# Performance work log

Measured on AMD Instinct MI355X. Metric: run time of the kernel, lower is better.

## Reference

```python
import jax, jax.numpy as jnp
import numpy as np

N_NODES = 100000
N_EDGES = 1600000
IN_DIM = 128
HIDDEN = 128
N_GRAPHS = 256


def setup_inputs() -> dict:
    key = jax.random.key(0)
    ks = jax.random.split(key, 12)
    x = jax.random.normal(ks[0], (N_NODES, IN_DIM), dtype=jnp.float32)
    edge_index = jax.random.randint(ks[1], (2, N_EDGES), 0, N_NODES, dtype=jnp.int64)
    batch = jnp.sort(jax.random.randint(ks[2], (N_NODES,), 0, N_GRAPHS, dtype=jnp.int64))
    s = 0.05
    W1 = jax.random.normal(ks[3], (IN_DIM, HIDDEN), dtype=jnp.float32) * s
    b1 = jnp.zeros((HIDDEN,), dtype=jnp.float32)
    W2 = jax.random.normal(ks[4], (HIDDEN, HIDDEN), dtype=jnp.float32) * s
    b2 = jnp.zeros((HIDDEN,), dtype=jnp.float32)
    W3 = jax.random.normal(ks[5], (HIDDEN, HIDDEN), dtype=jnp.float32) * s
    b3 = jnp.zeros((HIDDEN,), dtype=jnp.float32)
    Wh = jax.random.normal(ks[6], (HIDDEN, 2), dtype=jnp.float32) * s
    bh = jnp.zeros((2,), dtype=jnp.float32)
    return {"x": x, "edge_index": edge_index, "batch": batch,
            "W1": W1, "b1": b1, "W2": W2, "b2": b2, "W3": W3, "b3": b3,
            "Wh": Wh, "bh": bh}


def _gcn_structure(edge_index, n_nodes):
    # PyG GCNConv default: add self-loops, symmetric deg^-1/2 normalization.
    loop = jnp.arange(n_nodes, dtype=edge_index.dtype)
    src = jnp.concatenate([edge_index[0], loop])  # message source j
    dst = jnp.concatenate([edge_index[1], loop])  # aggregate at i
    deg = jax.ops.segment_sum(jnp.ones_like(dst, dtype=jnp.float32), dst,
                              num_segments=n_nodes)
    dinv = jnp.where(deg > 0, jax.lax.rsqrt(deg), 0.0)
    norm = dinv[src] * dinv[dst]  # [E + N]
    return src, dst, norm


def _gcn_conv(x, W, b, src, dst, norm, n_nodes):
    h = x @ W  # dense transform first (PyG order)
    msg = h[src] * norm[:, None]  # gather + per-edge scale
    agg = jax.ops.segment_sum(msg, dst, num_segments=n_nodes)  # scatter-add
    return agg + b


def reference(x, edge_index, batch, W1, b1, W2, b2, W3, b3, Wh, bh):
    n = x.shape[0]
    src, dst, norm = _gcn_structure(edge_index, n)
    # dropout is a no-op in eval mode (training=False)
    h = jax.nn.relu(_gcn_conv(x, W1, b1, src, dst, norm, n))
    h = jax.nn.relu(_gcn_conv(h, W2, b2, src, dst, norm, n))
    h = jax.nn.relu(_gcn_conv(h, W3, b3, src, dst, norm, n))
    # global_mean_pool over graph ids
    sums = jax.ops.segment_sum(h, batch, num_segments=N_GRAPHS)
    cnts = jax.ops.segment_sum(jnp.ones((n,), dtype=h.dtype), batch,
                               num_segments=N_GRAPHS)
    pooled = sums / jnp.maximum(cnts, 1.0)[:, None]
    return pooled @ Wh + bh  # [N_GRAPHS, 2]
```

## Files before the change

kernel.cpp:

```cpp
#include <hip/hip_runtime.h>


#define D 128
#define NB_SHIFT 8
#define BCAP 8192
#define EPB 4096

typedef unsigned int uint;
typedef unsigned short ushort;
typedef __attribute__((ext_vector_type(8))) short short8;
typedef __attribute__((ext_vector_type(4))) float f32x4;

__device__ __forceinline__ ushort f2bf(float f) {
    uint u = __float_as_uint(f);
    uint r = (u + 0x7fffu + ((u >> 16) & 1u)) >> 16;
    return (ushort)r;
}
__device__ __forceinline__ float bf2f(ushort b) {
    return __uint_as_float(((uint)b) << 16);
}
__device__ __forceinline__ float q15f(uint q) {
    return __uint_as_float(0x30000000u | (q << 13));
}

__device__ __forceinline__ void async_cp16(const ushort* g, ushort* lds_uniform) {
    __builtin_amdgcn_global_load_lds(
        (const __attribute__((address_space(1))) unsigned int*)g,
        (__attribute__((address_space(3))) unsigned int*)lds_uniform,
        16, 0, 0);
}

__global__ __launch_bounds__(256) void k_bucketA(const int* __restrict__ src,
                                                 const int* __restrict__ dst, int E,
                                                 int nbk, int* __restrict__ gcur,
                                                 uint* __restrict__ arena) {
    __shared__ int hist[512];
    __shared__ int rbase[512];
    int t = threadIdx.x;
    int e0 = blockIdx.x * EPB;
    int e1 = min(e0 + EPB, E);
    for (int i = t; i < nbk; i += 256) hist[i] = 0;
    __syncthreads();
    for (int e = e0 + t; e < e1; e += 256)
        atomicAdd(&hist[dst[e] >> NB_SHIFT], 1);
    __syncthreads();
    for (int i = t; i < nbk; i += 256) {
        int c = hist[i];
        rbase[i] = (c > 0) ? atomicAdd(&gcur[i], c) : 0;
        hist[i] = 0;
    }
    __syncthreads();
    for (int e = e0 + t; e < e1; e += 256) {
        int d = dst[e];
        int s = src[e];
        int b = d >> NB_SHIFT;
        int pos = rbase[b] + atomicAdd(&hist[b], 1);
        if (pos < BCAP)
            arena[(size_t)b * BCAP + pos] =
                ((uint)(d & ((1 << NB_SHIFT) - 1)) << 17) | (uint)s;
    }
}

__global__ __launch_bounds__(256) void k_degB(const uint* __restrict__ arena,
                                              const int* __restrict__ gcur, int N,
                                              int* __restrict__ degi,
                                              float* __restrict__ dinv) {
    int b = blockIdx.x;
    int t = threadIdx.x;
    __shared__ int hist[256];
    hist[t] = 0;
    __syncthreads();
    int cnt = min(gcur[b], BCAP);
    const uint* seg = arena + (size_t)b * BCAP;
    for (int i = t; i < cnt; i += 256)
        atomicAdd(&hist[seg[i] >> 17], 1);
    __syncthreads();
    int node = (b << NB_SHIFT) + t;
    if (node < N) {
        int c = hist[t];
        degi[node] = c;
        dinv[node] = rsqrtf((float)(c + 1));
    }
}

__global__ void k_scan1(const int* __restrict__ cnt, int N, int* __restrict__ bsum) {
    __shared__ int sdata[256];
    int t = threadIdx.x;
    int base = blockIdx.x * 1024 + t * 4;
    int s = 0;
#pragma unroll
    for (int j = 0; j < 4; j++) { int i = base + j; if (i < N) s += cnt[i]; }
    sdata[t] = s; __syncthreads();
    for (int off = 128; off > 0; off >>= 1) {
        if (t < off) sdata[t] += sdata[t + off];
        __syncthreads();
    }
    if (t == 0) bsum[blockIdx.x] = sdata[0];
}

__global__ void k_scan2(int* __restrict__ bsum, int nb) {
    if (threadIdx.x == 0) {
        int run = 0;
        for (int b = 0; b < nb; b++) { int v = bsum[b]; bsum[b] = run; run += v; }
    }
}

__global__ void k_scan3(const int* __restrict__ cnt, int N, const int* __restrict__ bofs,
                        int* __restrict__ row_start, int E) {
    __shared__ int sdata[256];
    int t = threadIdx.x;
    int base = blockIdx.x * 1024 + t * 4;
    int v[4]; int s = 0;
#pragma unroll
    for (int j = 0; j < 4; j++) { int i = base + j; v[j] = (i < N) ? cnt[i] : 0; s += v[j]; }
    sdata[t] = s; __syncthreads();
    for (int off = 1; off < 256; off <<= 1) {
        int x = (t >= off) ? sdata[t - off] : 0;
        __syncthreads();
        sdata[t] += x;
        __syncthreads();
    }
    int excl = (t == 0) ? 0 : sdata[t - 1];
    int run = bofs[blockIdx.x] + excl;
#pragma unroll
    for (int j = 0; j < 4; j++) {
        int i = base + j;
        if (i < N) row_start[i] = run;
        run += v[j];
    }
    if (blockIdx.x == 0 && t == 0) row_start[N] = E;
}

__global__ __launch_bounds__(256) void k_bucketB(const uint* __restrict__ arena,
                                                 const int* __restrict__ gcur,
                                                 const int* __restrict__ row_start,
                                                 const float* __restrict__ dinv,
                                                 int N, uint* __restrict__ csr) {
    int b = blockIdx.x;
    int t = threadIdx.x;
    int n0 = b << NB_SHIFT;
    int nn = min(1 << NB_SHIFT, N - n0);
    __shared__ float sdinv[256];
    __shared__ int sstart[256];
    __shared__ int scur[256];
    __shared__ uint sout[BCAP];
    for (int i = t; i < nn; i += 256) {
        sdinv[i]  = dinv[n0 + i];
        sstart[i] = row_start[n0 + i];
        scur[i]   = 0;
    }
    __syncthreads();
    int cnt = min(gcur[b], BCAP);
    int csr0 = sstart[0];
    for (int i = t; i < cnt; i += 256) {
        uint en = arena[(size_t)b * BCAP + i];
        int dl = en >> 17;
        int s  = en & 0x1FFFF;
        float nrm = dinv[s] * sdinv[dl];
        uint q = ((__float_as_uint(nrm) + 0x1000u) >> 13) & 0x7FFFu;
        int pos = atomicAdd(&scur[dl], 1);
        sout[(sstart[dl] - csr0) + pos] = ((uint)s << 15) | q;
    }
    __syncthreads();
    for (int i = t; i < cnt; i += 256)
        csr[csr0 + i] = sout[i];
}

__global__ void k_wsplit3(const float* __restrict__ W1, const float* __restrict__ W2,
                          const float* __restrict__ W3, ushort* __restrict__ Wf) {
    int gidx = blockIdx.x * blockDim.x + threadIdx.x;
    if (gidx >= 3 * 32768) return;
    int which = gidx >> 15;
    int idx = gidx & 32767;
    const float* W = (which == 0) ? W1 : (which == 1) ? W2 : W3;
    int i  = idx & 7;
    int l  = (idx >> 3) & 63;
    int nt = (idx >> 9) & 7;
    int kt = (idx >> 12) & 3;
    int h  = idx >> 14;
    int k = kt * 32 + (l >> 4) * 8 + i;
    int n = nt * 16 + (l & 15);
    float w = W[k * D + n];
    ushort hi = f2bf(w);
    ushort v = (h == 0) ? hi : f2bf(w - bf2f(hi));
    Wf[gidx] = v;
}

template <bool AF32>
__global__ __launch_bounds__(256) void k_gemm(const void* __restrict__ Ain,
                                              const ushort* __restrict__ Wf,
                                              ushort* __restrict__ out, int N) {
    __shared__ ushort As[64 * D];
    int t = threadIdx.x;
    int rowb = blockIdx.x * 64;

    if (AF32) {
        const float* A = (const float*)Ain;
#pragma unroll
        for (int i = 0; i < 8; i++) {
            int u = i * 256 + t;
            int row = u >> 5, c4 = u & 31;
            int grow = rowb + row;
            float4 v = make_float4(0.f, 0.f, 0.f, 0.f);
            if (grow < N) v = *(const float4*)(A + (size_t)grow * D + c4 * 4);
            uint2 p;
            p.x = (uint)f2bf(v.x) | ((uint)f2bf(v.y) << 16);
            p.y = (uint)f2bf(v.z) | ((uint)f2bf(v.w) << 16);
            int byteoff = row * 256 + ((c4 * 8) ^ ((row & 7) << 4));
            *(uint2*)((char*)As + byteoff) = p;
        }
    } else {
        const ushort* A = (const ushort*)Ain;
#pragma unroll
        for (int i = 0; i < 4; i++) {
            int u = i * 256 + t;
            int row = u >> 4, cp = u & 15;
            int grow = rowb + row;
            if (grow >= N) grow = N - 1;
            int gc = cp ^ (row & 7);
            const ushort* gp = A + (size_t)grow * D + gc * 8;
            ushort* lb = As + (size_t)(i * 256 + (t & 192)) * 8;
            async_cp16(gp, lb);
        }
        asm volatile("s_waitcnt vmcnt(0)" ::: "memory");
    }
    __syncthreads();

    int wave = t >> 6, lane = t & 63;
    const short8* Wf8 = (const short8*)Wf;

    short8 bhi[2][4], blo[2][4];
#pragma unroll
    for (int j = 0; j < 2; j++) {
        int nt = wave * 2 + j;
#pragma unroll
        for (int kt = 0; kt < 4; kt++) {
            bhi[j][kt] = Wf8[(size_t)((0 * 4 + kt) * 8 + nt) * 64 + lane];
            blo[j][kt] = Wf8[(size_t)((1 * 4 + kt) * 8 + nt) * 64 + lane];
        }
    }

    f32x4 acc[4][2];
#pragma unroll
    for (int m = 0; m < 4; m++)
#pragma unroll
        for (int j = 0; j < 2; j++) acc[m][j] = (f32x4){0.f, 0.f, 0.f, 0.f};

#pragma unroll
    for (int m = 0; m < 4; m++) {
        int r = m * 16 + (lane & 15);
#pragma unroll
        for (int kt = 0; kt < 4; kt++) {
            int raw = kt * 64 + (lane >> 4) * 16;
            short8 a = *(const short8*)((const char*)As + r * 256 + (raw ^ ((r & 7) << 4)));
#pragma unroll
            for (int j = 0; j < 2; j++) {
                acc[m][j] = __builtin_amdgcn_mfma_f32_16x16x32_bf16(a, bhi[j][kt], acc[m][j], 0, 0, 0);
                acc[m][j] = __builtin_amdgcn_mfma_f32_16x16x32_bf16(a, blo[j][kt], acc[m][j], 0, 0, 0);
            }
        }
    }

#pragma unroll
    for (int m = 0; m < 4; m++) {
#pragma unroll
        for (int j = 0; j < 2; j++) {
            int colb = (wave * 2 + j) * 16 + (lane & 15);
#pragma unroll
            for (int jj = 0; jj < 4; jj++) {
                int grow = rowb + m * 16 + (lane >> 4) * 4 + jj;
                if (grow < N)
                    out[(size_t)grow * D + colb] = f2bf(acc[m][j][jj]);
            }
        }
    }
}

__device__ __forceinline__ void agg_core(const ushort* __restrict__ T,
                                         const uint* __restrict__ csr,
                                         int beg, int end, int col,
                                         float& a0, float& a1) {
    if (beg >= end) return;
    int lane16 = threadIdx.x & 15;
    uint cur = csr[min(beg + lane16, end - 1)];
    for (int e = beg; e < end; e += 16) {
        uint nxt = 0;
        int en = e + 16;
        if (en < end) nxt = csr[min(en + lane16, end - 1)];
        uint v[16];
        float nn[16];
#pragma unroll
        for (int q = 0; q < 16; q++) {
            uint c = __builtin_amdgcn_readlane(cur, q);
            nn[q] = (e + q < end) ? q15f(c & 0x7FFFu) : 0.f;
            v[q] = *(const uint*)(T + (size_t)(c >> 15) * D + col);
        }
#pragma unroll
        for (int q = 0; q < 16; q++) {
            a0 = fmaf(nn[q], __uint_as_float(v[q] << 16), a0);
            a1 = fmaf(nn[q], __uint_as_float(v[q] & 0xffff0000u), a1);
        }
        cur = nxt;
    }
}

__global__ __launch_bounds__(256) void k_agg(const ushort* __restrict__ T,
                                             const float* __restrict__ dinv,
                                             const int* __restrict__ row_start,
                                             const uint* __restrict__ csr,
                                             const float* __restrict__ bias,
                                             ushort* __restrict__ out, int N) {
    int node = __builtin_amdgcn_readfirstlane(blockIdx.x * 4 + (threadIdx.x >> 6));
    if (node >= N) return;
    int lane = threadIdx.x & 63;
    int col = lane * 2;

    float di = dinv[node];
    uint vs = *(const uint*)(T + (size_t)node * D + col);
    float sw = di * di;
    float a0 = sw * __uint_as_float(vs << 16);
    float a1 = sw * __uint_as_float(vs & 0xffff0000u);

    agg_core(T, csr, row_start[node], row_start[node + 1], col, a0, a1);

    a0 = fmaxf(a0 + bias[col], 0.f);
    a1 = fmaxf(a1 + bias[col + 1], 0.f);
    ushort2 o; o.x = f2bf(a0); o.y = f2bf(a1);
    *(ushort2*)(out + (size_t)node * D + col) = o;
}

__global__ __launch_bounds__(256) void k_agg_head(const ushort* __restrict__ T,
                                                  const float* __restrict__ dinv,
                                                  const int* __restrict__ row_start,
                                                  const uint* __restrict__ csr,
                                                  const float* __restrict__ bias,
                                                  const float* __restrict__ Wh,
                                                  float2* __restrict__ y, int N) {
    int node = __builtin_amdgcn_readfirstlane(blockIdx.x * 4 + (threadIdx.x >> 6));
    if (node >= N) return;
    int lane = threadIdx.x & 63;
    int col = lane * 2;

    float di = dinv[node];
    uint vs = *(const uint*)(T + (size_t)node * D + col);
    float sw = di * di;
    float a0 = sw * __uint_as_float(vs << 16);
    float a1 = sw * __uint_as_float(vs & 0xffff0000u);

    agg_core(T, csr, row_start[node], row_start[node + 1], col, a0, a1);

    a0 = fmaxf(a0 + bias[col], 0.f);
    a1 = fmaxf(a1 + bias[col + 1], 0.f);

    float p0 = a0 * Wh[col * 2 + 0] + a1 * Wh[(col + 1) * 2 + 0];
    float p1 = a0 * Wh[col * 2 + 1] + a1 * Wh[(col + 1) * 2 + 1];
#pragma unroll
    for (int off = 32; off > 0; off >>= 1) {
        p0 += __shfl_xor(p0, off);
        p1 += __shfl_xor(p1, off);
    }
    if (lane == 0) y[node] = make_float2(p0, p1);
}

__global__ __launch_bounds__(256) void k_pool2(const float2* __restrict__ y,
                                               const int* __restrict__ batch, int N,
                                               const float* __restrict__ bh,
                                               float* __restrict__ out) {
    int g = blockIdx.x;
    int t = threadIdx.x;
    int lo = 0, hi = N;
    while (lo < hi) { int m = (lo + hi) >> 1; if (batch[m] < g) lo = m + 1; else hi = m; }
    int beg = lo;
    lo = 0; hi = N;
    while (lo < hi) { int m = (lo + hi) >> 1; if (batch[m] < g + 1) lo = m + 1; else hi = m; }
    int endi = lo;

    float s0 = 0.f, s1 = 0.f;
    for (int i = beg + t; i < endi; i += 256) {
        float2 v = y[i];
        s0 += v.x; s1 += v.y;
    }
    __shared__ float r0[256], r1[256];
    r0[t] = s0; r1[t] = s1;
    __syncthreads();
    for (int off = 128; off > 0; off >>= 1) {
        if (t < off) { r0[t] += r0[t + off]; r1[t] += r1[t + off]; }
        __syncthreads();
    }
    if (t == 0) {
        float cnt = (float)((endi - beg) > 0 ? (endi - beg) : 1);
        out[g * 2 + 0] = r0[0] / cnt + bh[0];
        out[g * 2 + 1] = r1[0] / cnt + bh[1];
    }
}

extern "C" void kernel_launch(void* const* d_in, const int* in_sizes, int n_in,
                              void* d_out, int out_size, void* d_ws, size_t ws_size,
                              hipStream_t stream) {
    const float* x   = (const float*)d_in[0];
    const int* eidx  = (const int*)d_in[1];
    const int* batch = (const int*)d_in[2];
    const float* W1 = (const float*)d_in[3];
    const float* b1 = (const float*)d_in[4];
    const float* W2 = (const float*)d_in[5];
    const float* b2 = (const float*)d_in[6];
    const float* W3 = (const float*)d_in[7];
    const float* b3 = (const float*)d_in[8];
    const float* Wh = (const float*)d_in[9];
    const float* bh = (const float*)d_in[10];

    int E = in_sizes[1] / 2;
    int N = in_sizes[2];
    int ngraphs = out_size / 2;
    const int* src = eidx;
    const int* dst = eidx + E;
    int nbk = (N + (1 << NB_SHIFT) - 1) >> NB_SHIFT;

    char* ws = (char*)d_ws;
    size_t off = 0;
    auto alloc = [&](size_t bytes) -> void* {
        void* p = ws + off;
        off = (off + bytes + 255) & ~(size_t)255;
        return p;
    };
    ushort* Hbf      = (ushort*)alloc((size_t)N * D * 2);
    ushort* T        = (ushort*)alloc((size_t)N * D * 2);
    ushort* Wf       = (ushort*)alloc(3 * 32768 * 2);
    int*    degi     = (int*)alloc((size_t)N * 4);
    float*  dinv     = (float*)alloc((size_t)N * 4);
    int*    row_start= (int*)alloc((size_t)(N + 1) * 4);
    int*    gcur     = (int*)alloc((size_t)nbk * 4);
    int*    bofs     = (int*)alloc(4096);
    float2* y        = (float2*)alloc((size_t)N * 8);
    uint*   csr      = (uint*)alloc((size_t)E * 4);
    uint*   arena    = (uint*)alloc((size_t)nbk * BCAP * 4);
    (void)ws_size;

    hipMemsetAsync(gcur, 0, (size_t)nbk * 4, stream);

    k_bucketA<<<(E + EPB - 1) / EPB, 256, 0, stream>>>(src, dst, E, nbk, gcur, arena);
    k_degB<<<nbk, 256, 0, stream>>>(arena, gcur, N, degi, dinv);

    int nb = (N + 1023) / 1024;
    k_scan1<<<nb, 256, 0, stream>>>(degi, N, bofs);
    k_scan2<<<1, 64, 0, stream>>>(bofs, nb);
    k_scan3<<<nb, 256, 0, stream>>>(degi, N, bofs, row_start, E);

    k_bucketB<<<nbk, 256, 0, stream>>>(arena, gcur, row_start, dinv, N, csr);

    k_wsplit3<<<384, 256, 0, stream>>>(W1, W2, W3, Wf);

    int gemm_grid = (N + 63) / 64;
    int agg_grid = (N + 3) / 4;

    k_gemm<true><<<gemm_grid, 256, 0, stream>>>(x, Wf, T, N);
    k_agg<<<agg_grid, 256, 0, stream>>>(T, dinv, row_start, csr, b1, Hbf, N);
    k_gemm<false><<<gemm_grid, 256, 0, stream>>>(Hbf, Wf + 32768, T, N);
    k_agg<<<agg_grid, 256, 0, stream>>>(T, dinv, row_start, csr, b2, Hbf, N);
    k_gemm<false><<<gemm_grid, 256, 0, stream>>>(Hbf, Wf + 65536, T, N);
    k_agg_head<<<agg_grid, 256, 0, stream>>>(T, dinv, row_start, csr, b3, Wh, y, N);
    k_pool2<<<ngraphs, 256, 0, stream>>>(y, batch, N, bh, (float*)d_out);
}
```

Baseline: 307.9 us.

## Fuse edge bucketing with first GEMM and replace three-pass scan

Merges the edge-bucketing kernel and the first dense GEMM into one launch whose blocks split by index, so the two independent stages can run concurrently on the GPU. It also replaces the three-kernel global degree scan with a single-block scan over per-bucket counts plus a per-bucket local scan inside the degree kernel, which computes row_start directly. This removes several small launches and the degi array, at the cost of sharing LDS sizing between the two roles in the merged kernel.

```diff
diff --git a/kernel.cpp b/kernel.cpp
--- a/kernel.cpp
+++ b/kernel.cpp
@@ -30,14 +30,13 @@
         16, 0, 0);
 }
 
-__global__ __launch_bounds__(256) void k_bucketA(const int* __restrict__ src,
-                                                 const int* __restrict__ dst, int E,
-                                                 int nbk, int* __restrict__ gcur,
-                                                 uint* __restrict__ arena) {
-    __shared__ int hist[512];
-    __shared__ int rbase[512];
-    int t = threadIdx.x;
-    int e0 = blockIdx.x * EPB;
+__device__ __forceinline__ void bucketA_body(const int* __restrict__ src,
+                                             const int* __restrict__ dst, int E,
+                                             int nbk, int* __restrict__ gcur,
+                                             uint* __restrict__ arena, int bid,
+                                             int* hist, int* rbase) {
+    int t = threadIdx.x;
+    int e0 = bid * EPB;
     int e1 = min(e0 + EPB, E);
     for (int i = t; i < nbk; i += 256) hist[i] = 0;
     __syncthreads();
@@ -61,13 +60,145 @@
     }
 }
 
-__global__ __launch_bounds__(256) void k_degB(const uint* __restrict__ arena,
-                                              const int* __restrict__ gcur, int N,
-                                              int* __restrict__ degi,
-                                              float* __restrict__ dinv) {
+template <bool AF32>
+__device__ __forceinline__ void gemm_body(const void* __restrict__ Ain,
+                                          const ushort* __restrict__ Wf,
+                                          ushort* __restrict__ out, int N,
+                                          int rowb, ushort* As) {
+    int t = threadIdx.x;
+
+    if (AF32) {
+        const float* A = (const float*)Ain;
+#pragma unroll
+        for (int i = 0; i < 8; i++) {
+            int u = i * 256 + t;
+            int row = u >> 5, c4 = u & 31;
+            int grow = rowb + row;
+            float4 v = make_float4(0.f, 0.f, 0.f, 0.f);
+            if (grow < N) v = *(const float4*)(A + (size_t)grow * D + c4 * 4);
+            uint2 p;
+            p.x = (uint)f2bf(v.x) | ((uint)f2bf(v.y) << 16);
+            p.y = (uint)f2bf(v.z) | ((uint)f2bf(v.w) << 16);
+            int byteoff = row * 256 + ((c4 * 8) ^ ((row & 7) << 4));
+            *(uint2*)((char*)As + byteoff) = p;
+        }
+    } else {
+        const ushort* A = (const ushort*)Ain;
+#pragma unroll
+        for (int i = 0; i < 4; i++) {
+            int u = i * 256 + t;
+            int row = u >> 4, cp = u & 15;
+            int grow = rowb + row;
+            if (grow >= N) grow = N - 1;
+            int gc = cp ^ (row & 7);
+            const ushort* gp = A + (size_t)grow * D + gc * 8;
+            ushort* lb = As + (size_t)(i * 256 + (t & 192)) * 8;
+            async_cp16(gp, lb);
+        }
+        asm volatile("s_waitcnt vmcnt(0)" ::: "memory");
+    }
+    __syncthreads();
+
+    int wave = t >> 6, lane = t & 63;
+    const short8* Wf8 = (const short8*)Wf;
+
+    short8 bhi[2][4], blo[2][4];
+#pragma unroll
+    for (int j = 0; j < 2; j++) {
+        int nt = wave * 2 + j;
+#pragma unroll
+        for (int kt = 0; kt < 4; kt++) {
+            bhi[j][kt] = Wf8[(size_t)((0 * 4 + kt) * 8 + nt) * 64 + lane];
+            blo[j][kt] = Wf8[(size_t)((1 * 4 + kt) * 8 + nt) * 64 + lane];
+        }
+    }
+
+    f32x4 acc[4][2];
+#pragma unroll
+    for (int m = 0; m < 4; m++)
+#pragma unroll
+        for (int j = 0; j < 2; j++) acc[m][j] = (f32x4){0.f, 0.f, 0.f, 0.f};
+
+#pragma unroll
+    for (int m = 0; m < 4; m++) {
+        int r = m * 16 + (lane & 15);
+#pragma unroll
+        for (int kt = 0; kt < 4; kt++) {
+            int raw = kt * 64 + (lane >> 4) * 16;
+            short8 a = *(const short8*)((const char*)As + r * 256 + (raw ^ ((r & 7) << 4)));
+#pragma unroll
+            for (int j = 0; j < 2; j++) {
+                acc[m][j] = __builtin_amdgcn_mfma_f32_16x16x32_bf16(a, bhi[j][kt], acc[m][j], 0, 0, 0);
+                acc[m][j] = __builtin_amdgcn_mfma_f32_16x16x32_bf16(a, blo[j][kt], acc[m][j], 0, 0, 0);
+            }
+        }
+    }
+
+#pragma unroll
+    for (int m = 0; m < 4; m++) {
+#pragma unroll
+        for (int j = 0; j < 2; j++) {
+            int colb = (wave * 2 + j) * 16 + (lane & 15);
+#pragma unroll
+            for (int jj = 0; jj < 4; jj++) {
+                int grow = rowb + m * 16 + (lane >> 4) * 4 + jj;
+                if (grow < N)
+                    out[(size_t)grow * D + colb] = f2bf(acc[m][j][jj]);
+            }
+        }
+    }
+}
+
+__global__ __launch_bounds__(256) void k_build_gemm1(const int* __restrict__ src,
+                                                     const int* __restrict__ dst, int E,
+                                                     int nbk, int* __restrict__ gcur,
+                                                     uint* __restrict__ arena, int nA,
+                                                     const float* __restrict__ x,
+                                                     const ushort* __restrict__ Wf,
+                                                     ushort* __restrict__ T, int N) {
+    __shared__ ushort As[64 * D];
+    if ((int)blockIdx.x < nA) {
+        int* hist = (int*)As;
+        int* rbase = hist + 512;
+        bucketA_body(src, dst, E, nbk, gcur, arena, blockIdx.x, hist, rbase);
+    } else {
+        gemm_body<true>(x, Wf, T, N, (blockIdx.x - nA) * 64, As);
+    }
+}
+
+template <bool AF32>
+__global__ __launch_bounds__(256) void k_gemm(const void* __restrict__ Ain,
+                                              const ushort* __restrict__ Wf,
+                                              ushort* __restrict__ out, int N) {
+    __shared__ ushort As[64 * D];
+    gemm_body<AF32>(Ain, Wf, out, N, blockIdx.x * 64, As);
+}
+
+__global__ void k_scanG(const int* __restrict__ gcur, int nbk, int E,
+                        int* __restrict__ bbase, int* __restrict__ row_start, int N) {
+    __shared__ int s[512];
+    int t = threadIdx.x;
+    s[t] = (t < nbk) ? gcur[t] : 0;
+    __syncthreads();
+    for (int off = 1; off < 512; off <<= 1) {
+        int x = (t >= off) ? s[t - off] : 0;
+        __syncthreads();
+        s[t] += x;
+        __syncthreads();
+    }
+    if (t < nbk) bbase[t] = s[t] - gcur[t];
+    if (t == 0) row_start[N] = E;
+}
+
+__global__ __launch_bounds__(256) void k_degB2(const uint* __restrict__ arena,
+                                               const int* __restrict__ gcur,
+                                               const int* __restrict__ bbase, int N,
+                                               float* __restrict__ dinv,
+                                               int* __restrict__ row_start) {
     int b = blockIdx.x;
     int t = threadIdx.x;
     __shared__ int hist[256];
+    __shared__ int sc[256];
     hist[t] = 0;
     __syncthreads();
     int cnt = min(gcur[b], BCAP);
@@ -75,60 +206,20 @@
     for (int i = t; i < cnt; i += 256)
         atomicAdd(&hist[seg[i] >> 17], 1);
     __syncthreads();
+    int c = hist[t];
+    sc[t] = c;
+    __syncthreads();
+    for (int off = 1; off < 256; off <<= 1) {
+        int x = (t >= off) ? sc[t - off] : 0;
+        __syncthreads();
+        sc[t] += x;
+        __syncthreads();
+    }
     int node = (b << NB_SHIFT) + t;
     if (node < N) {
-        int c = hist[t];
-        degi[node] = c;
         dinv[node] = rsqrtf((float)(c + 1));
-    }
-}
-
-__global__ void k_scan1(const int* __restrict__ cnt, int N, int* __restrict__ bsum) {
-    __shared__ int sdata[256];
-    int t = threadIdx.x;
-    int base = blockIdx.x * 1024 + t * 4;
-    int s = 0;
-#pragma unroll
-    for (int j = 0; j < 4; j++) { int i = base + j; if (i < N) s += cnt[i]; }
-    sdata[t] = s; __syncthreads();
-    for (int off = 128; off > 0; off >>= 1) {
-        if (t < off) sdata[t] += sdata[t + off];
-        __syncthreads();
-    }
-    if (t == 0) bsum[blockIdx.x] = sdata[0];
-}
-
-__global__ void k_scan2(int* __restrict__ bsum, int nb) {
-    if (threadIdx.x == 0) {
-        int run = 0;
-        for (int b = 0; b < nb; b++) { int v = bsum[b]; bsum[b] = run; run += v; }
-    }
-}
-
-__global__ void k_scan3(const int* __restrict__ cnt, int N, const int* __restrict__ bofs,
-                        int* __restrict__ row_start, int E) {
-    __shared__ int sdata[256];
-    int t = threadIdx.x;
-    int base = blockIdx.x * 1024 + t * 4;
-    int v[4]; int s = 0;
-#pragma unroll
-    for (int j = 0; j < 4; j++) { int i = base + j; v[j] = (i < N) ? cnt[i] : 0; s += v[j]; }
-    sdata[t] = s; __syncthreads();
-    for (int off = 1; off < 256; off <<= 1) {
-        int x = (t >= off) ? sdata[t - off] : 0;
-        __syncthreads();
-        sdata[t] += x;
-        __syncthreads();
-    }
-    int excl = (t == 0) ? 0 : sdata[t - 1];
-    int run = bofs[blockIdx.x] + excl;
-#pragma unroll
-    for (int j = 0; j < 4; j++) {
-        int i = base + j;
-        if (i < N) row_start[i] = run;
-        run += v[j];
-    }
-    if (blockIdx.x == 0 && t == 0) row_start[N] = E;
+        row_start[node] = bbase[b] + sc[t] - c;
+    }
 }
 
 __global__ __launch_bounds__(256) void k_bucketB(const uint* __restrict__ arena,
@@ -186,96 +277,6 @@
     Wf[gidx] = v;
 }
 
-template <bool AF32>
-__global__ __launch_bounds__(256) void k_gemm(const void* __restrict__ Ain,
-                                              const ushort* __restrict__ Wf,
-                                              ushort* __restrict__ out, int N) {
-    __shared__ ushort As[64 * D];
-    int t = threadIdx.x;
-    int rowb = blockIdx.x * 64;
-
-    if (AF32) {
-        const float* A = (const float*)Ain;
-#pragma unroll
-        for (int i = 0; i < 8; i++) {
-            int u = i * 256 + t;
-            int row = u >> 5, c4 = u & 31;
-            int grow = rowb + row;
-            float4 v = make_float4(0.f, 0.f, 0.f, 0.f);
-            if (grow < N) v = *(const float4*)(A + (size_t)grow * D + c4 * 4);
-            uint2 p;
-            p.x = (uint)f2bf(v.x) | ((uint)f2bf(v.y) << 16);
-            p.y = (uint)f2bf(v.z) | ((uint)f2bf(v.w) << 16);
-            int byteoff = row * 256 + ((c4 * 8) ^ ((row & 7) << 4));
-            *(uint2*)((char*)As + byteoff) = p;
-        }
-    } else {
-        const ushort* A = (const ushort*)Ain;
-#pragma unroll
-        for (int i = 0; i < 4; i++) {
-            int u = i * 256 + t;
-            int row = u >> 4, cp = u & 15;
-            int grow = rowb + row;
-            if (grow >= N) grow = N - 1;
-            int gc = cp ^ (row & 7);
-            const ushort* gp = A + (size_t)grow * D + gc * 8;
-            ushort* lb = As + (size_t)(i * 256 + (t & 192)) * 8;
-            async_cp16(gp, lb);
-        }
-        asm volatile("s_waitcnt vmcnt(0)" ::: "memory");
-    }
-    __syncthreads();
-
-    int wave = t >> 6, lane = t & 63;
-    const short8* Wf8 = (const short8*)Wf;
-
-    short8 bhi[2][4], blo[2][4];
-#pragma unroll
-    for (int j = 0; j < 2; j++) {
-        int nt = wave * 2 + j;
-#pragma unroll
-        for (int kt = 0; kt < 4; kt++) {
-            bhi[j][kt] = Wf8[(size_t)((0 * 4 + kt) * 8 + nt) * 64 + lane];
-            blo[j][kt] = Wf8[(size_t)((1 * 4 + kt) * 8 + nt) * 64 + lane];
-        }
-    }
-
-    f32x4 acc[4][2];
-#pragma unroll
-    for (int m = 0; m < 4; m++)
-#pragma unroll
-        for (int j = 0; j < 2; j++) acc[m][j] = (f32x4){0.f, 0.f, 0.f, 0.f};
-
-#pragma unroll
-    for (int m = 0; m < 4; m++) {
-        int r = m * 16 + (lane & 15);
-#pragma unroll
-        for (int kt = 0; kt < 4; kt++) {
-            int raw = kt * 64 + (lane >> 4) * 16;
-            short8 a = *(const short8*)((const char*)As + r * 256 + (raw ^ ((r & 7) << 4)));
-#pragma unroll
-            for (int j = 0; j < 2; j++) {
-                acc[m][j] = __builtin_amdgcn_mfma_f32_16x16x32_bf16(a, bhi[j][kt], acc[m][j], 0, 0, 0);
-                acc[m][j] = __builtin_amdgcn_mfma_f32_16x16x32_bf16(a, blo[j][kt], acc[m][j], 0, 0, 0);
-            }
-        }
-    }
-
-#pragma unroll
-    for (int m = 0; m < 4; m++) {
-#pragma unroll
-        for (int j = 0; j < 2; j++) {
-            int colb = (wave * 2 + j) * 16 + (lane & 15);
-#pragma unroll
-            for (int jj = 0; jj < 4; jj++) {
-                int grow = rowb + m * 16 + (lane >> 4) * 4 + jj;
-                if (grow < N)
-                    out[(size_t)grow * D + colb] = f2bf(acc[m][j][jj]);
-            }
-        }
-    }
-}
-
 __device__ __forceinline__ void agg_core(const ushort* __restrict__ T,
                                          const uint* __restrict__ csr,
                                          int beg, int end, int col,
@@ -426,34 +427,28 @@
     ushort* Hbf      = (ushort*)alloc((size_t)N * D * 2);
     ushort* T        = (ushort*)alloc((size_t)N * D * 2);
     ushort* Wf       = (ushort*)alloc(3 * 32768 * 2);
-    int*    degi     = (int*)alloc((size_t)N * 4);
     float*  dinv     = (float*)alloc((size_t)N * 4);
     int*    row_start= (int*)alloc((size_t)(N + 1) * 4);
     int*    gcur     = (int*)alloc((size_t)nbk * 4);
-    int*    bofs     = (int*)alloc(4096);
+    int*    bbase    = (int*)alloc((size_t)nbk * 4);
     float2* y        = (float2*)alloc((size_t)N * 8);
     uint*   csr      = (uint*)alloc((size_t)E * 4);
     uint*   arena    = (uint*)alloc((size_t)nbk * BCAP * 4);
     (void)ws_size;
 
     hipMemsetAsync(gcur, 0, (size_t)nbk * 4, stream);
-
-    k_bucketA<<<(E + EPB - 1) / EPB, 256, 0, stream>>>(src, dst, E, nbk, gcur, arena);
-    k_degB<<<nbk, 256, 0, stream>>>(arena, gcur, N, degi, dinv);
-
-    int nb = (N + 1023) / 1024;
-    k_scan1<<<nb, 256, 0, stream>>>(degi, N, bofs);
-    k_scan2<<<1, 64, 0, stream>>>(bofs, nb);
-    k_scan3<<<nb, 256, 0, stream>>>(degi, N, bofs, row_start, E);
-
-    k_bucketB<<<nbk, 256, 0, stream>>>(arena, gcur, row_start, dinv, N, csr);
-
     k_wsplit3<<<384, 256, 0, stream>>>(W1, W2, W3, Wf);
 
     int gemm_grid = (N + 63) / 64;
     int agg_grid = (N + 3) / 4;
-
-    k_gemm<true><<<gemm_grid, 256, 0, stream>>>(x, Wf, T, N);
+    int nA = (E + EPB - 1) / EPB;
+
+    k_build_gemm1<<<nA + gemm_grid, 256, 0, stream>>>(src, dst, E, nbk, gcur, arena,
+                                                      nA, x, Wf, T, N);
+    k_scanG<<<1, 512, 0, stream>>>(gcur, nbk, E, bbase, row_start, N);
+    k_degB2<<<nbk, 256, 0, stream>>>(arena, gcur, bbase, N, dinv, row_start);
+    k_bucketB<<<nbk, 256, 0, stream>>>(arena, gcur, row_start, dinv, N, csr);
+
     k_agg<<<agg_grid, 256, 0, stream>>>(T, dinv, row_start, csr, b1, Hbf, N);
     k_gemm<false><<<gemm_grid, 256, 0, stream>>>(Hbf, Wf + 32768, T, N);
     k_agg<<<agg_grid, 256, 0, stream>>>(T, dinv, row_start, csr, b2, Hbf, N);
```

Measured after the change: 289.2 us. 1.06x faster.
